# Kernel optimization log

Measured on AMD Instinct MI355X. Metric: run time of the kernel, lower is better.

The kernel has to match this reference:

```python
import jax, jax.numpy as jnp
import numpy as np
import math

BS, S, DIM, H = 2, 2048, 1024, 16
DH = DIM // H


def setup_inputs() -> dict:
    key = jax.random.key(0)
    ks = jax.random.split(key, 11)
    std = 1.0 / math.sqrt(DIM)
    inp = {
        "query": jax.random.normal(ks[0], (BS, S, DIM), jnp.float32),
        "key_": jax.random.normal(ks[1], (BS, S, DIM), jnp.float32),
        "value": jax.random.normal(ks[2], (BS, S, DIM), jnp.float32),
        "mask": jnp.ones((BS, S), jnp.int32),
        "q_w": jax.random.normal(ks[3], (DIM, DIM), jnp.float32) * std,
        "q_b": jnp.zeros((DIM,), jnp.float32),
        "k_w": jax.random.normal(ks[4], (DIM, DIM), jnp.float32) * std,
        "k_b": jnp.zeros((DIM,), jnp.float32),
        "v_w": jax.random.normal(ks[5], (DIM, DIM), jnp.float32) * std,
        "v_b": jnp.zeros((DIM,), jnp.float32),
        "o_w": jax.random.normal(ks[6], (DIM, DIM), jnp.float32) * std,
        "o_b": jnp.zeros((DIM,), jnp.float32),
    }
    return inp


def _shape(x):
    # (bs, s, dim) -> (bs, h, s, dh)
    return x.reshape(BS, -1, H, DH).transpose(0, 2, 1, 3)


def reference(query, key_, value, mask, q_w, q_b, k_w, k_b, v_w, v_b, o_w, o_b):
    # linear projections (torch Linear: x @ W.T + b)
    q = _shape(query @ q_w.T + q_b) / math.sqrt(DH)
    k = _shape(key_ @ k_w.T + k_b)
    v = _shape(value @ v_w.T + v_b)
    # scores: (bs, h, s, s)
    scores = jnp.einsum("bhqd,bhkd->bhqk", q, k)
    pad = (mask == 0)[:, None, None, :]  # (bs,1,1,k_len)
    scores = jnp.where(pad, -jnp.inf, scores)
    weights = jax.nn.softmax(scores, axis=-1)
    context = jnp.einsum("bhqk,bhkd->bhqd", weights, v)
    context = context.transpose(0, 2, 1, 3).reshape(BS, -1, DIM)
    return context @ o_w.T + o_b
```

## Files before the change

### kernel.cpp

```cpp
#include <hip/hip_runtime.h>
#include <hip/hip_bf16.h>

#define BSZ 2
#define SEQ 2048
#define DIMN 1024
#define NH 16
#define DH 64
#define LOG2E 1.4426950408889634f

typedef unsigned short ushort_t;
typedef __attribute__((ext_vector_type(8))) short short8;
typedef __attribute__((ext_vector_type(4))) float float4v;

__device__ __forceinline__ ushort_t f2bf(float f) {
    union { float f; unsigned int u; } c; c.f = f;
    return (ushort_t)((c.u + 0x8000u) >> 16);
}
__device__ __forceinline__ unsigned int pkbf(float a, float b) {
    __hip_bfloat162 h = __float22bfloat162_rn(make_float2(a, b));
    unsigned int u; __builtin_memcpy(&u, &h, 4); return u;
}

__global__ __launch_bounds__(256) void cvt_w(
    const float* __restrict__ w0, const float* __restrict__ w1,
    const float* __restrict__ w2, const float* __restrict__ w3,
    ushort_t* __restrict__ o0, ushort_t* __restrict__ o1,
    ushort_t* __restrict__ o2, ushort_t* __restrict__ o3)
{
    const float* s; ushort_t* d;
    switch (blockIdx.y) {
        case 0: s = w0; d = o0; break;
        case 1: s = w1; d = o1; break;
        case 2: s = w2; d = o2; break;
        default: s = w3; d = o3; break;
    }
    int i = (blockIdx.x * 256 + threadIdx.x) * 4;
    float4v v = *(const float4v*)(s + i);
    uint2 o; o.x = pkbf(v[0], v[1]); o.y = pkbf(v[2], v[3]);
    *(uint2*)(d + i) = o;
}

__global__ __launch_bounds__(256) void gemm_qkv(
    const float* __restrict__ xq, const float* __restrict__ xk, const float* __restrict__ xv,
    const ushort_t* __restrict__ Wq, const ushort_t* __restrict__ Wk, const ushort_t* __restrict__ Wv,
    const float* __restrict__ qb, const float* __restrict__ kb, const float* __restrict__ vb,
    ushort_t* __restrict__ Qp, ushort_t* __restrict__ Kp, ushort_t* __restrict__ VpT)
{
    __shared__ ushort_t As[128 * 72];
    __shared__ ushort_t Bs[128 * 72];
    const int tid  = threadIdx.x;
    const int lane = tid & 63;
    const int w    = tid >> 6;
    const int wm   = w >> 1, wn = w & 1;
    const int quad = lane >> 4;
    const int l16  = lane & 15;
    const int mBase = blockIdx.y * 128;
    const int nGlob = blockIdx.x * 128;
    const int z     = nGlob >> 10;
    const int nBase = nGlob & 1023;
    const float*    A    = (z == 0) ? xq : (z == 1) ? xk : xv;
    const ushort_t* W    = (z == 0) ? Wq : (z == 1) ? Wk : Wv;
    const float*    bias = (z == 0) ? qb : (z == 1) ? kb : vb;

    float4v acc[4][4];
    const float4v z4 = {0.f, 0.f, 0.f, 0.f};
#pragma unroll
    for (int i = 0; i < 4; ++i)
#pragma unroll
        for (int j = 0; j < 4; ++j) acc[i][j] = z4;

    for (int k0 = 0; k0 < 1024; k0 += 64) {
        float4v a[4][2];
        short8  wb[4];
#pragma unroll
        for (int it = 0; it < 4; ++it) {
            int c = it * 256 + tid, row = c >> 3, col = (c & 7) * 8;
            const float* g = A + (size_t)(mBase + row) * 1024 + k0 + col;
            a[it][0] = *(const float4v*)g;
            a[it][1] = *(const float4v*)(g + 4);
            wb[it] = *(const short8*)(W + (size_t)(nBase + row) * 1024 + k0 + col);
        }
        __syncthreads();
#pragma unroll
        for (int it = 0; it < 4; ++it) {
            int c = it * 256 + tid, row = c >> 3, col = (c & 7) * 8;
            uint4 ua;
            ua.x = pkbf(a[it][0][0], a[it][0][1]); ua.y = pkbf(a[it][0][2], a[it][0][3]);
            ua.z = pkbf(a[it][1][0], a[it][1][1]); ua.w = pkbf(a[it][1][2], a[it][1][3]);
            *(uint4*)&As[row * 72 + col] = ua;
            *(short8*)&Bs[row * 72 + col] = wb[it];
        }
        __syncthreads();

#pragma unroll
        for (int ksub = 0; ksub < 2; ++ksub) {
            short8 af[4], bf[4];
#pragma unroll
            for (int mt = 0; mt < 4; ++mt)
                af[mt] = *(const short8*)&As[(wm * 64 + mt * 16 + l16) * 72 + ksub * 32 + quad * 8];
#pragma unroll
            for (int nt = 0; nt < 4; ++nt)
                bf[nt] = *(const short8*)&Bs[(wn * 64 + nt * 16 + l16) * 72 + ksub * 32 + quad * 8];
#pragma unroll
            for (int mt = 0; mt < 4; ++mt)
#pragma unroll
                for (int nt = 0; nt < 4; ++nt)
                    acc[mt][nt] = __builtin_amdgcn_mfma_f32_16x16x32_bf16(af[mt], bf[nt], acc[mt][nt], 0, 0, 0);
        }
    }

    const float scale = (z == 0) ? 0.125f * LOG2E : 1.0f;
    if (z < 2) {
        ushort_t* C = (z == 0) ? Qp : Kp;
#pragma unroll
        for (int mt = 0; mt < 4; ++mt)
#pragma unroll
            for (int nt = 0; nt < 4; ++nt) {
                int colg = nBase + wn * 64 + nt * 16 + l16;
                float bv = bias[colg];
#pragma unroll
                for (int r = 0; r < 4; ++r) {
                    int rowg = mBase + wm * 64 + mt * 16 + quad * 4 + r;
                    C[(size_t)rowg * 1024 + colg] = f2bf((acc[mt][nt][r] + bv) * scale);
                }
            }
    } else {
#pragma unroll
        for (int mt = 0; mt < 4; ++mt)
#pragma unroll
            for (int nt = 0; nt < 4; ++nt) {
                int n = nBase + wn * 64 + nt * 16 + l16;
                int hh = n >> 6, d = n & 63;
                float bv = bias[n];
                int rowg = mBase + wm * 64 + mt * 16 + quad * 4;
                int b = rowg >> 11, s = rowg & 2047;
                uint2 pk;
                pk.x = pkbf(acc[mt][nt][0] + bv, acc[mt][nt][1] + bv);
                pk.y = pkbf(acc[mt][nt][2] + bv, acc[mt][nt][3] + bv);
                *(uint2*)&VpT[(((size_t)(b * 16 + hh) * 64 + d) << 11) + s] = pk;
            }
    }
}

__global__ __launch_bounds__(256) void gemm_o(
    const ushort_t* __restrict__ A, const ushort_t* __restrict__ W,
    const float* __restrict__ bias, float* __restrict__ C)
{
    __shared__ ushort_t As[128 * 72];
    __shared__ ushort_t Bs[64 * 72];
    const int tid  = threadIdx.x;
    const int lane = tid & 63;
    const int w    = tid >> 6;
    const int wm   = w & 1, wn = w >> 1;
    const int quad = lane >> 4;
    const int l16  = lane & 15;
    const int mBase = blockIdx.y * 128;
    const int nBase = blockIdx.x * 64;

    float4v acc[4][2];
    const float4v z4 = {0.f, 0.f, 0.f, 0.f};
#pragma unroll
    for (int mt = 0; mt < 4; ++mt)
#pragma unroll
        for (int nt = 0; nt < 2; ++nt) acc[mt][nt] = z4;

    for (int k0 = 0; k0 < 1024; k0 += 64) {
        short8 ab[4], wb[2];
#pragma unroll
        for (int it = 0; it < 4; ++it) {
            int c = it * 256 + tid, row = c >> 3, col = (c & 7) * 8;
            ab[it] = *(const short8*)(A + (size_t)(mBase + row) * 1024 + k0 + col);
        }
#pragma unroll
        for (int it = 0; it < 2; ++it) {
            int c = it * 256 + tid, row = c >> 3, col = (c & 7) * 8;
            wb[it] = *(const short8*)(W + (size_t)(nBase + row) * 1024 + k0 + col);
        }
        __syncthreads();
#pragma unroll
        for (int it = 0; it < 4; ++it) {
            int c = it * 256 + tid, row = c >> 3, col = (c & 7) * 8;
            *(short8*)&As[row * 72 + col] = ab[it];
        }
#pragma unroll
        for (int it = 0; it < 2; ++it) {
            int c = it * 256 + tid, row = c >> 3, col = (c & 7) * 8;
            *(short8*)&Bs[row * 72 + col] = wb[it];
        }
        __syncthreads();

#pragma unroll
        for (int ksub = 0; ksub < 2; ++ksub) {
            short8 af[4], bf[2];
#pragma unroll
            for (int mt = 0; mt < 4; ++mt)
                af[mt] = *(const short8*)&As[(wm * 64 + mt * 16 + l16) * 72 + ksub * 32 + quad * 8];
#pragma unroll
            for (int nt = 0; nt < 2; ++nt)
                bf[nt] = *(const short8*)&Bs[(wn * 32 + nt * 16 + l16) * 72 + ksub * 32 + quad * 8];
#pragma unroll
            for (int mt = 0; mt < 4; ++mt)
#pragma unroll
                for (int nt = 0; nt < 2; ++nt)
                    acc[mt][nt] = __builtin_amdgcn_mfma_f32_16x16x32_bf16(af[mt], bf[nt], acc[mt][nt], 0, 0, 0);
        }
    }

#pragma unroll
    for (int mt = 0; mt < 4; ++mt)
#pragma unroll
        for (int nt = 0; nt < 2; ++nt) {
            int colg = nBase + wn * 32 + nt * 16 + l16;
            float bv = bias[colg];
#pragma unroll
            for (int r = 0; r < 4; ++r) {
                int rowg = mBase + wm * 64 + mt * 16 + quad * 4 + r;
                C[(size_t)rowg * 1024 + colg] = acc[mt][nt][r] + bv;
            }
        }
}

__global__ __launch_bounds__(512) void attn_kernel(
    const ushort_t* __restrict__ Qp, const ushort_t* __restrict__ Kp,
    const ushort_t* __restrict__ VpT, const int* __restrict__ mask,
    ushort_t* __restrict__ Cp)
{
    __shared__ ushort_t QPs[128 * 72];
    __shared__ ushort_t Ks[2][64 * 72];
    __shared__ ushort_t Vt[2][64 * 72];
    __shared__ int s_mok[8];

    const int tid  = threadIdx.x;
    const int lane = tid & 63;
    const int w    = tid >> 6;
    const int quad = lane >> 4;
    const int l16  = lane & 15;
    const int b    = blockIdx.x >> 4;
    const int h    = blockIdx.x & 15;
    const int q0   = blockIdx.y * 128;

    const int srow = tid >> 3, scol = (tid & 7) * 8;
    const ushort_t* Vbase = VpT + ((size_t)(b * 16 + h) * 64) * 2048;
    const ushort_t* Kbase = Kp + (size_t)b * SEQ * DIMN + h * DH;

    {
        int m0 = mask[b * SEQ + tid];
        int m1 = mask[b * SEQ + 512 + tid];
        int m2 = mask[b * SEQ + 1024 + tid];
        int m3 = mask[b * SEQ + 1536 + tid];
        int ok = __all((m0 != 0) & (m1 != 0) & (m2 != 0) & (m3 != 0));
        if (lane == 0) s_mok[w] = ok;
    }

    short8 qreg[2];
#pragma unroll
    for (int it = 0; it < 2; ++it) {
        int c = it * 512 + tid, row = c >> 3, col = (c & 7) * 8;
        qreg[it] = *(const short8*)(Qp + (size_t)(b * SEQ + q0 + row) * DIMN + h * DH + col);
    }
    short8 kreg = *(const short8*)(Kbase + (size_t)srow * DIMN + scol);
    short8 vreg = *(const short8*)(Vbase + (size_t)srow * 2048 + scol);
#pragma unroll
    for (int it = 0; it < 2; ++it) {
        int c = it * 512 + tid, row = c >> 3, col = (c & 7) * 8;
        *(short8*)&QPs[row * 72 + col] = qreg[it];
    }
    *(short8*)&Ks[0][srow * 72 + scol] = kreg;
    *(short8*)&Vt[0][srow * 72 + scol] = vreg;
    kreg = *(const short8*)(Kbase + (size_t)(64 + srow) * DIMN + scol);
    vreg = *(const short8*)(Vbase + (size_t)srow * 2048 + 64 + scol);
    __syncthreads();

    const int mall = s_mok[0] & s_mok[1] & s_mok[2] & s_mok[3]
                   & s_mok[4] & s_mok[5] & s_mok[6] & s_mok[7];

    short8 bq[2];
#pragma unroll
    for (int ks = 0; ks < 2; ++ks)
        bq[ks] = *(const short8*)&QPs[(w * 16 + l16) * 72 + ks * 32 + quad * 8];

    const float4v z4 = {0.f, 0.f, 0.f, 0.f};
    float4v Oacc[4];
#pragma unroll
    for (int vt = 0; vt < 4; ++vt) Oacc[vt] = z4;
    float4v Lacc = z4;
    float mrow = -3e38f;

    short8 ones;
#pragma unroll
    for (int j = 0; j < 8; ++j) ones[j] = (short)0x3F80;

    for (int it = 0; it < SEQ / 64; ++it) {
        const int bsel = it & 1;
        const int kt0  = it * 64;

        if (it + 1 < SEQ / 64) {
            *(short8*)&Ks[bsel ^ 1][srow * 72 + scol] = kreg;
            *(short8*)&Vt[bsel ^ 1][srow * 72 + scol] = vreg;
        }
        if (it + 2 < SEQ / 64) {
            int kn = kt0 + 128;
            kreg = *(const short8*)(Kbase + (size_t)(kn + srow) * DIMN + scol);
            vreg = *(const short8*)(Vbase + (size_t)srow * 2048 + kn + scol);
        }

        float4v Sv[4];
#pragma unroll
        for (int kt = 0; kt < 4; ++kt) Sv[kt] = z4;
        __builtin_amdgcn_s_setprio(1);
#pragma unroll
        for (int ks = 0; ks < 2; ++ks)
#pragma unroll
            for (int kt = 0; kt < 4; ++kt) {
                short8 ak = *(const short8*)&Ks[bsel][(kt * 16 + l16) * 72 + ks * 32 + quad * 8];
                Sv[kt] = __builtin_amdgcn_mfma_f32_16x16x32_bf16(ak, bq[ks], Sv[kt], 0, 0, 0);
            }
        __builtin_amdgcn_s_setprio(0);

        if (!mall) {
            int4 mv4[4];
#pragma unroll
            for (int kt = 0; kt < 4; ++kt)
                mv4[kt] = *(const int4*)(mask + b * SEQ + kt0 + kt * 16 + quad * 4);
#pragma unroll
            for (int kt = 0; kt < 4; ++kt) {
                int4 mv = mv4[kt];
#pragma unroll
                for (int r = 0; r < 4; ++r) {
                    int m = (r == 0) ? mv.x : (r == 1) ? mv.y : (r == 2) ? mv.z : mv.w;
                    Sv[kt][r] += (m == 0) ? -1e30f : 0.0f;
                }
            }
        }

        float mx = Sv[0][0];
#pragma unroll
        for (int kt = 0; kt < 4; ++kt)
#pragma unroll
            for (int r = 0; r < 4; ++r) mx = fmaxf(mx, Sv[kt][r]);
        mx = fmaxf(mx, __shfl_xor(mx, 16));
        mx = fmaxf(mx, __shfl_xor(mx, 32));
        if (!__all(mx - mrow <= 8.0f)) {
            float mn = fmaxf(mrow, mx);
            float alpha = exp2f(mrow - mn);
            mrow = mn;
#pragma unroll
            for (int vt = 0; vt < 4; ++vt) Oacc[vt] *= alpha;
            Lacc *= alpha;
        }
#pragma unroll
        for (int kt = 0; kt < 4; ++kt)
#pragma unroll
            for (int r = 0; r < 4; ++r) Sv[kt][r] = exp2f(Sv[kt][r] - mrow);

#pragma unroll
        for (int kt = 0; kt < 4; ++kt) {
            uint2 pk;
            pk.x = pkbf(Sv[kt][0], Sv[kt][1]);
            pk.y = pkbf(Sv[kt][2], Sv[kt][3]);
            *(uint2*)&QPs[(w * 16 + l16) * 72 + kt * 16 + quad * 4] = pk;
        }

        __builtin_amdgcn_s_setprio(1);
#pragma unroll
        for (int ks = 0; ks < 2; ++ks) {
            short8 bp = *(const short8*)&QPs[(w * 16 + l16) * 72 + ks * 32 + quad * 8];
            Lacc = __builtin_amdgcn_mfma_f32_16x16x32_bf16(ones, bp, Lacc, 0, 0, 0);
#pragma unroll
            for (int vt = 0; vt < 4; ++vt) {
                short8 av = *(const short8*)&Vt[bsel][(vt * 16 + l16) * 72 + ks * 32 + quad * 8];
                Oacc[vt] = __builtin_amdgcn_mfma_f32_16x16x32_bf16(av, bp, Oacc[vt], 0, 0, 0);
            }
        }
        __builtin_amdgcn_s_setprio(0);

        __syncthreads();
    }

    float inv = 1.0f / Lacc[0];
    int row = q0 + w * 16 + l16;
#pragma unroll
    for (int vt = 0; vt < 4; ++vt) {
        uint2 pk;
        pk.x = pkbf(Oacc[vt][0] * inv, Oacc[vt][1] * inv);
        pk.y = pkbf(Oacc[vt][2] * inv, Oacc[vt][3] * inv);
        *(uint2*)&Cp[(size_t)(b * SEQ + row) * DIMN + h * DH + vt * 16 + quad * 4] = pk;
    }
}

extern "C" void kernel_launch(void* const* d_in, const int* in_sizes, int n_in,
                              void* d_out, int out_size, void* d_ws, size_t ws_size,
                              hipStream_t stream) {
    const float* x_q = (const float*)d_in[0];
    const float* x_k = (const float*)d_in[1];
    const float* x_v = (const float*)d_in[2];
    const int*   msk = (const int*)d_in[3];
    const float* q_w = (const float*)d_in[4];
    const float* q_b = (const float*)d_in[5];
    const float* k_w = (const float*)d_in[6];
    const float* k_b = (const float*)d_in[7];
    const float* v_w = (const float*)d_in[8];
    const float* v_b = (const float*)d_in[9];
    const float* o_w = (const float*)d_in[10];
    const float* o_b = (const float*)d_in[11];
    float* out = (float*)d_out;

    const size_t NEL = (size_t)BSZ * SEQ * DIMN;
    const size_t WEL = (size_t)DIMN * DIMN;
    ushort_t* Qp  = (ushort_t*)d_ws;
    ushort_t* Kp  = Qp + NEL;
    ushort_t* VpT = Kp + NEL;
    ushort_t* Wq  = VpT + NEL;
    ushort_t* Wk  = Wq + WEL;
    ushort_t* Wv  = Wk + WEL;
    ushort_t* Wo  = Wv + WEL;
    ushort_t* Cp  = Qp;

    cvt_w<<<dim3(WEL / 1024, 4), 256, 0, stream>>>(q_w, k_w, v_w, o_w, Wq, Wk, Wv, Wo);
    gemm_qkv<<<dim3(24, 32), 256, 0, stream>>>(x_q, x_k, x_v, Wq, Wk, Wv,
                                               q_b, k_b, v_b, Qp, Kp, VpT);
    attn_kernel<<<dim3(BSZ * NH, SEQ / 128), 512, 0, stream>>>(Qp, Kp, VpT, msk, Cp);
    gemm_o<<<dim3(16, 32), 256, 0, stream>>>(Cp, Wo, o_b, out);
}
```

Baseline: 264.1 us.

## Load attention tiles via global_load_lds with XOR-swizzled LDS and fold max-subtraction into MFMA

Replaces the register-staged K/V/Q global loads and padded LDS tiles with direct global-to-LDS 16-byte loads into unpadded 64-wide tiles. Bank conflicts are avoided with an XOR swizzle on the 8-element chunk index. The running-max subtraction moves into the QK MFMA accumulator init (mneg4), so the per-element subtract before exp2 disappears except when the max is rescaled. The prefetch distance shrinks from two tiles to one, and the change depends on global_load_lds completing before the loop barrier.

After: 261.1 us. Within noise of the previous version (-1.1%).

```diff
diff --git a/kernel.cpp b/kernel.cpp
--- a/kernel.cpp
+++ b/kernel.cpp
@@ -19,6 +19,11 @@
 __device__ __forceinline__ unsigned int pkbf(float a, float b) {
     __hip_bfloat162 h = __float22bfloat162_rn(make_float2(a, b));
     unsigned int u; __builtin_memcpy(&u, &h, 4); return u;
+}
+__device__ __forceinline__ void gld16(const ushort_t* g, ushort_t* l) {
+    __builtin_amdgcn_global_load_lds(
+        (const __attribute__((address_space(1))) unsigned int*)g,
+        (__attribute__((address_space(3))) unsigned int*)l, 16, 0, 0);
 }
 
 __global__ __launch_bounds__(256) void cvt_w(
@@ -225,9 +230,9 @@
     const ushort_t* __restrict__ VpT, const int* __restrict__ mask,
     ushort_t* __restrict__ Cp)
 {
-    __shared__ ushort_t QPs[128 * 72];
-    __shared__ ushort_t Ks[2][64 * 72];
-    __shared__ ushort_t Vt[2][64 * 72];
+    __shared__ __align__(16) ushort_t Qs[128 * 64];
+    __shared__ __align__(16) ushort_t Ks[2][64 * 64];
+    __shared__ __align__(16) ushort_t Vt[2][64 * 64];
     __shared__ int s_mok[8];
 
     const int tid  = threadIdx.x;
@@ -235,13 +240,17 @@
     const int w    = tid >> 6;
     const int quad = lane >> 4;
     const int l16  = lane & 15;
+    const int sw   = l16 & 7;
     const int b    = blockIdx.x >> 4;
     const int h    = blockIdx.x & 15;
     const int q0   = blockIdx.y * 128;
 
-    const int srow = tid >> 3, scol = (tid & 7) * 8;
+    const int srow = tid >> 3;
+    const int sc   = tid & 7;
+    const int gsc  = (sc ^ (srow & 7)) * 8;
     const ushort_t* Vbase = VpT + ((size_t)(b * 16 + h) * 64) * 2048;
     const ushort_t* Kbase = Kp + (size_t)b * SEQ * DIMN + h * DH;
+    const ushort_t* Qbase = Qp + (size_t)(b * SEQ + q0) * DIMN + h * DH;
 
     {
         int m0 = mask[b * SEQ + tid];
@@ -252,23 +261,14 @@
         if (lane == 0) s_mok[w] = ok;
     }
 
-    short8 qreg[2];
-#pragma unroll
-    for (int it = 0; it < 2; ++it) {
-        int c = it * 512 + tid, row = c >> 3, col = (c & 7) * 8;
-        qreg[it] = *(const short8*)(Qp + (size_t)(b * SEQ + q0 + row) * DIMN + h * DH + col);
-    }
-    short8 kreg = *(const short8*)(Kbase + (size_t)srow * DIMN + scol);
-    short8 vreg = *(const short8*)(Vbase + (size_t)srow * 2048 + scol);
-#pragma unroll
-    for (int it = 0; it < 2; ++it) {
-        int c = it * 512 + tid, row = c >> 3, col = (c & 7) * 8;
-        *(short8*)&QPs[row * 72 + col] = qreg[it];
-    }
-    *(short8*)&Ks[0][srow * 72 + scol] = kreg;
-    *(short8*)&Vt[0][srow * 72 + scol] = vreg;
-    kreg = *(const short8*)(Kbase + (size_t)(64 + srow) * DIMN + scol);
-    vreg = *(const short8*)(Vbase + (size_t)srow * 2048 + 64 + scol);
+#pragma unroll
+    for (int it2 = 0; it2 < 2; ++it2) {
+        int row = it2 * 64 + srow;
+        gld16(Qbase + (size_t)row * DIMN + ((sc ^ (row & 7)) * 8),
+              &Qs[(it2 * 64 + w * 8) * 64]);
+    }
+    gld16(Kbase + (size_t)srow * DIMN + gsc, &Ks[0][w * 512]);
+    gld16(Vbase + (size_t)srow * 2048 + gsc, &Vt[0][w * 512]);
     __syncthreads();
 
     const int mall = s_mok[0] & s_mok[1] & s_mok[2] & s_mok[3]
@@ -277,44 +277,43 @@
     short8 bq[2];
 #pragma unroll
     for (int ks = 0; ks < 2; ++ks)
-        bq[ks] = *(const short8*)&QPs[(w * 16 + l16) * 72 + ks * 32 + quad * 8];
+        bq[ks] = *(const short8*)&Qs[(w * 16 + l16) * 64 + ((4 * ks + quad) ^ sw) * 8];
 
     const float4v z4 = {0.f, 0.f, 0.f, 0.f};
     float4v Oacc[4];
 #pragma unroll
     for (int vt = 0; vt < 4; ++vt) Oacc[vt] = z4;
     float4v Lacc = z4;
-    float mrow = -3e38f;
+    float mrow = 0.0f;
+    float4v mneg4 = z4;
 
     short8 ones;
 #pragma unroll
     for (int j = 0; j < 8; ++j) ones[j] = (short)0x3F80;
 
-    for (int it = 0; it < SEQ / 64; ++it) {
+    const int NT = SEQ / 64;
+    for (int it = 0; it < NT; ++it) {
         const int bsel = it & 1;
         const int kt0  = it * 64;
 
-        if (it + 1 < SEQ / 64) {
-            *(short8*)&Ks[bsel ^ 1][srow * 72 + scol] = kreg;
-            *(short8*)&Vt[bsel ^ 1][srow * 72 + scol] = vreg;
-        }
-        if (it + 2 < SEQ / 64) {
-            int kn = kt0 + 128;
-            kreg = *(const short8*)(Kbase + (size_t)(kn + srow) * DIMN + scol);
-            vreg = *(const short8*)(Vbase + (size_t)srow * 2048 + kn + scol);
+        if (it + 1 < NT) {
+            int kn = kt0 + 64;
+            gld16(Kbase + (size_t)(kn + srow) * DIMN + gsc, &Ks[bsel ^ 1][w * 512]);
+            gld16(Vbase + (size_t)srow * 2048 + kn + gsc, &Vt[bsel ^ 1][w * 512]);
         }
 
         float4v Sv[4];
-#pragma unroll
-        for (int kt = 0; kt < 4; ++kt) Sv[kt] = z4;
         __builtin_amdgcn_s_setprio(1);
 #pragma unroll
-        for (int ks = 0; ks < 2; ++ks)
-#pragma unroll
-            for (int kt = 0; kt < 4; ++kt) {
-                short8 ak = *(const short8*)&Ks[bsel][(kt * 16 + l16) * 72 + ks * 32 + quad * 8];
-                Sv[kt] = __builtin_amdgcn_mfma_f32_16x16x32_bf16(ak, bq[ks], Sv[kt], 0, 0, 0);
-            }
+        for (int kt = 0; kt < 4; ++kt) {
+            short8 ak = *(const short8*)&Ks[bsel][(kt * 16 + l16) * 64 + (quad ^ sw) * 8];
+            Sv[kt] = __builtin_amdgcn_mfma_f32_16x16x32_bf16(ak, bq[0], mneg4, 0, 0, 0);
+        }
+#pragma unroll
+        for (int kt = 0; kt < 4; ++kt) {
+            short8 ak = *(const short8*)&Ks[bsel][(kt * 16 + l16) * 64 + ((4 + quad) ^ sw) * 8];
+            Sv[kt] = __builtin_amdgcn_mfma_f32_16x16x32_bf16(ak, bq[1], Sv[kt], 0, 0, 0);
+        }
         __builtin_amdgcn_s_setprio(0);
 
         if (!mall) {
@@ -333,42 +332,48 @@
             }
         }
 
-        float mx = Sv[0][0];
-#pragma unroll
-        for (int kt = 0; kt < 4; ++kt)
-#pragma unroll
-            for (int r = 0; r < 4; ++r) mx = fmaxf(mx, Sv[kt][r]);
+        float t0 = fmaxf(fmaxf(Sv[0][0], Sv[0][1]), fmaxf(Sv[0][2], Sv[0][3]));
+        float t1 = fmaxf(fmaxf(Sv[1][0], Sv[1][1]), fmaxf(Sv[1][2], Sv[1][3]));
+        float t2 = fmaxf(fmaxf(Sv[2][0], Sv[2][1]), fmaxf(Sv[2][2], Sv[2][3]));
+        float t3 = fmaxf(fmaxf(Sv[3][0], Sv[3][1]), fmaxf(Sv[3][2], Sv[3][3]));
+        float mx = fmaxf(fmaxf(t0, t1), fmaxf(t2, t3));
         mx = fmaxf(mx, __shfl_xor(mx, 16));
         mx = fmaxf(mx, __shfl_xor(mx, 32));
-        if (!__all(mx - mrow <= 8.0f)) {
-            float mn = fmaxf(mrow, mx);
-            float alpha = exp2f(mrow - mn);
-            mrow = mn;
+        if (!__all(mx <= 8.0f)) {
+            float d = fmaxf(mx, 0.0f);
+            float alpha = exp2f(-d);
+            mrow += d;
 #pragma unroll
             for (int vt = 0; vt < 4; ++vt) Oacc[vt] *= alpha;
             Lacc *= alpha;
+#pragma unroll
+            for (int kt = 0; kt < 4; ++kt)
+#pragma unroll
+                for (int r = 0; r < 4; ++r) Sv[kt][r] -= d;
+            mneg4[0] = -mrow; mneg4[1] = -mrow; mneg4[2] = -mrow; mneg4[3] = -mrow;
         }
 #pragma unroll
         for (int kt = 0; kt < 4; ++kt)
 #pragma unroll
-            for (int r = 0; r < 4; ++r) Sv[kt][r] = exp2f(Sv[kt][r] - mrow);
+            for (int r = 0; r < 4; ++r) Sv[kt][r] = exp2f(Sv[kt][r]);
 
 #pragma unroll
         for (int kt = 0; kt < 4; ++kt) {
             uint2 pk;
             pk.x = pkbf(Sv[kt][0], Sv[kt][1]);
             pk.y = pkbf(Sv[kt][2], Sv[kt][3]);
-            *(uint2*)&QPs[(w * 16 + l16) * 72 + kt * 16 + quad * 4] = pk;
+            int chunk = (2 * kt + (quad >> 1)) ^ sw;
+            *(uint2*)&Qs[(w * 16 + l16) * 64 + chunk * 8 + (quad & 1) * 4] = pk;
         }
 
         __builtin_amdgcn_s_setprio(1);
 #pragma unroll
         for (int ks = 0; ks < 2; ++ks) {
-            short8 bp = *(const short8*)&QPs[(w * 16 + l16) * 72 + ks * 32 + quad * 8];
+            short8 bp = *(const short8*)&Qs[(w * 16 + l16) * 64 + ((4 * ks + quad) ^ sw) * 8];
             Lacc = __builtin_amdgcn_mfma_f32_16x16x32_bf16(ones, bp, Lacc, 0, 0, 0);
 #pragma unroll
             for (int vt = 0; vt < 4; ++vt) {
-                short8 av = *(const short8*)&Vt[bsel][(vt * 16 + l16) * 72 + ks * 32 + quad * 8];
+                short8 av = *(const short8*)&Vt[bsel][(vt * 16 + l16) * 64 + ((4 * ks + quad) ^ sw) * 8];
                 Oacc[vt] = __builtin_amdgcn_mfma_f32_16x16x32_bf16(av, bp, Oacc[vt], 0, 0, 0);
             }
         }
```
